# Kernel optimization log

Measured on AMD Instinct MI355X. Metric: run time of the kernel, lower is better.

Reference implementation:

```python
import jax, jax.numpy as jnp
import numpy as np

N_LOC, CONTENT, ADDR, HID, IN, OUT = 32768, 512, 64, 1024, 256, 10
OVERALL = CONTENT + ADDR   # 576
GRU_IN = IN + OVERALL      # 832
EPS = 1e-7


def setup_inputs() -> dict:
    key = jax.random.key(0)
    ks = jax.random.split(key, 16)
    def w(i, shape, scale=0.02):
        return jax.random.normal(ks[i], shape, jnp.float32) * scale
    return {
        "x": jax.random.normal(ks[0], (IN, 1), jnp.float32),
        "h0": jnp.zeros((HID, 1), jnp.float32),
        "memory_contents": w(1, (N_LOC, CONTENT)),
        "memory_addresses": w(2, (N_LOC, ADDR)),
        "W_query": w(3, (OVERALL, HID)),
        "b_query": jnp.zeros((OVERALL, 1), jnp.float32),
        "u_sharpen": w(4, (1, HID)),
        "b_sharpen": jnp.zeros((1, 1), jnp.float32),
        "u_lru": w(5, (1, HID)),
        "b_lru": jnp.zeros((1, 1), jnp.float32),
        "W_erase": w(6, (CONTENT, HID)),
        "b_erase": jnp.zeros((CONTENT, 1), jnp.float32),
        "W_content_hidden": w(7, (CONTENT, HID)),
        "W_content_input": w(8, (CONTENT, IN)),
        "b_content": jnp.zeros((CONTENT, 1), jnp.float32),
        "W_ih": w(9, (3 * HID, GRU_IN)),
        "W_hh": w(10, (3 * HID, HID)),
        "b_ih": jnp.zeros((3 * HID,), jnp.float32),
        "b_hh": jnp.zeros((3 * HID,), jnp.float32),
        "W_output": w(11, (OUT, HID)),
        "b_output": jnp.zeros((OUT, 1), jnp.float32),
        "num_addressing_steps": 8,
    }


def _dntm_forward(x, h0, memory_contents, memory_addresses, W_query, b_query,
                  u_sharpen, b_sharpen, u_lru, b_lru, W_erase, b_erase,
                  W_content_hidden, W_content_input, b_content,
                  W_ih, W_hh, b_ih, b_hh, W_output, b_output, num_steps):
    addr_norm_sq = jnp.sum(memory_addresses * memory_addresses, axis=1)  # (N,) constant across steps
    xcol = x[:, 0]

    def step(carry, _):
        h, mem, ema = carry  # h: (HID,1), mem: (N,CONTENT), ema: (N,)
        # --- address memory (content-based, sharpened, LRU-gated) ---
        query = (W_query @ h + b_query)[:, 0]                        # (OVERALL,)
        beta = jax.nn.softplus(u_sharpen @ h + b_sharpen)[0, 0] + 1.0
        full = jnp.concatenate([mem, memory_addresses], axis=1)      # (N, OVERALL) full memory view
        dots = full @ query                                          # (N,)
        row_norm = jnp.sqrt(jnp.sum(mem * mem, axis=1) + addr_norm_sq)
        sim = beta * dots / (row_norm * jnp.linalg.norm(query) + EPS)  # sharpened cosine sim (N,)
        gamma = jax.nn.sigmoid(u_lru @ h + b_lru)[0, 0]
        w_addr = jax.nn.softmax(sim - gamma * ema)                   # (N,)
        ema_new = 0.1 * ema + 0.9 * sim
        # --- read ---
        reading = full.T @ w_addr                                    # (OVERALL,)
        # --- GRU controller step (torch GRUCell math) ---
        gi = W_ih @ jnp.concatenate([xcol, reading]) + b_ih          # (3*HID,)
        gh = W_hh @ h[:, 0] + b_hh
        r = jax.nn.sigmoid(gi[:HID] + gh[:HID])
        z = jax.nn.sigmoid(gi[HID:2 * HID] + gh[HID:2 * HID])
        n = jnp.tanh(gi[2 * HID:] + r * gh[2 * HID:])
        h_new = ((1.0 - z) * n + z * h[:, 0])[:, None]               # (HID,1)
        # --- write/update memory: rank-1 erase + rank-1 add ---
        erase = jax.nn.sigmoid(W_erase @ h_new + b_erase)[:, 0]      # (CONTENT,)
        cand = jax.nn.relu(W_content_hidden @ h_new + W_content_input @ x + b_content)[:, 0]
        mem_new = mem * (1.0 - w_addr[:, None] * erase[None, :]) + w_addr[:, None] * cand[None, :]
        return (h_new, mem_new, ema_new), None

    ema0 = jnp.zeros((N_LOC,), memory_contents.dtype)
    (h, _, _), _ = jax.lax.scan(step, (h0, memory_contents, ema0), None, length=num_steps)
    output = jax.nn.log_softmax(W_output @ h + b_output, axis=0)     # (OUT,1)
    return h, output


def reference(x, h0, memory_contents, memory_addresses, W_query, b_query,
              u_sharpen, b_sharpen, u_lru, b_lru, W_erase, b_erase,
              W_content_hidden, W_content_input, b_content,
              W_ih, W_hh, b_ih, b_hh, W_output, b_output, num_addressing_steps):
    return _dntm_forward(x, h0, memory_contents, memory_addresses, W_query, b_query,
                         u_sharpen, b_sharpen, u_lru, b_lru, W_erase, b_erase,
                         W_content_hidden, W_content_input, b_content,
                         W_ih, W_hh, b_ih, b_hh, W_output, b_output, num_addressing_steps)
```

## Files before the change

kernel.cpp:

```cpp
#include <hip/hip_runtime.h>
#include <math.h>

#define N_LOC 32768
#define CONTENT 512
#define ADDR_D 64
#define HID 1024
#define IN_D 256
#define OUT_D 10
#define OVERALL 576
#define GRU_IN 832
#define EPS_C 1e-7f
#define NSTEPS 8

#define NBLK_P 2048
#define NWAVE_P (NBLK_P * 4)
#define RCOLS (OVERALL + 1)
#define RP 580
#define NRED 32

__device__ __forceinline__ float wred(float v) {
    #pragma unroll
    for (int m = 32; m; m >>= 1) v += __shfl_xor(v, m, 64);
    return v;
}
__device__ __forceinline__ float sigm(float x) { return 1.0f / (1.0f + expf(-x)); }
__device__ __forceinline__ float dot4(float4 a, float4 b) {
    return a.x * b.x + a.y * b.y + a.z * b.z + a.w * b.w;
}

__global__ __launch_bounds__(256) void k_init(const float* __restrict__ addrRows,
                                              float* __restrict__ addrsq,
                                              float* __restrict__ ema) {
    int tid = threadIdx.x, wid = tid >> 6, lane = tid & 63;
    int gid = blockIdx.x * 256 + tid;
    if (gid < N_LOC) ema[gid] = 0.0f;
    for (int i = blockIdx.x * 4 + wid; i < N_LOC; i += gridDim.x * 4) {
        float a = addrRows[(size_t)i * ADDR_D + lane];
        float sq = wred(a * a);
        if (lane == 0) addrsq[i] = sq;
    }
}

__global__ __launch_bounds__(256) void k_small(
    const float* __restrict__ W_e, const float* __restrict__ b_e,
    const float* __restrict__ W_ch, const float* __restrict__ W_ci, const float* __restrict__ b_c,
    const float* __restrict__ W_q, const float* __restrict__ b_q,
    const float* __restrict__ u_s, const float* __restrict__ u_l,
    const float* __restrict__ x, const float* __restrict__ h,
    float* __restrict__ erase, float* __restrict__ cand, float* __restrict__ query,
    float* __restrict__ slots_t, int doEC) {
    int tid = threadIdx.x, wid = tid >> 6, lane = tid & 63;
    int t = blockIdx.x * 4 + wid;
    const int base = doEC ? 2 * CONTENT : 0;
    const float4* h4 = (const float4*)h;
    const float4* x4 = (const float4*)x;
    if (doEC && t < CONTENT) {
        const float4* row = (const float4*)(W_e + (size_t)t * HID);
        float d = 0.0f;
        #pragma unroll
        for (int i = 0; i < 4; i++) d += dot4(row[lane + 64 * i], h4[lane + 64 * i]);
        d = wred(d);
        if (lane == 0) erase[t] = sigm(d + b_e[t]);
    } else if (doEC && t < 2 * CONTENT) {
        int r = t - CONTENT;
        const float4* row = (const float4*)(W_ch + (size_t)r * HID);
        float d = 0.0f;
        #pragma unroll
        for (int i = 0; i < 4; i++) d += dot4(row[lane + 64 * i], h4[lane + 64 * i]);
        const float4* row2 = (const float4*)(W_ci + (size_t)r * IN_D);
        d += dot4(row2[lane], x4[lane]);
        d = wred(d);
        if (lane == 0) cand[r] = fmaxf(d + b_c[r], 0.0f);
    } else if (t >= base && t < base + OVERALL) {
        int r = t - base;
        const float4* row = (const float4*)(W_q + (size_t)r * HID);
        float d = 0.0f;
        #pragma unroll
        for (int i = 0; i < 4; i++) d += dot4(row[lane + 64 * i], h4[lane + 64 * i]);
        d = wred(d);
        if (lane == 0) query[r] = d + b_q[r];
    } else if (t == base + OVERALL) {
        const float4* us4 = (const float4*)u_s;
        float d = 0.0f;
        #pragma unroll
        for (int i = 0; i < 4; i++) d += dot4(us4[lane + 64 * i], h4[lane + 64 * i]);
        d = wred(d);
        if (lane == 0) slots_t[1] = d;
    } else if (t == base + OVERALL + 1) {
        const float4* ul4 = (const float4*)u_l;
        float d = 0.0f;
        #pragma unroll
        for (int i = 0; i < 4; i++) d += dot4(ul4[lane + 64 * i], h4[lane + 64 * i]);
        d = wred(d);
        if (lane == 0) slots_t[2] = d;
    }
}

__global__ __launch_bounds__(256) void k_passAB(
    const float* __restrict__ memC,
    const float* __restrict__ addrRows, const float* __restrict__ query,
    const float* __restrict__ eraseAll, const float* __restrict__ candAll,
    const float* __restrict__ addrsq, float* __restrict__ ema,
    const float* __restrict__ expAll, float* __restrict__ exp_t,
    float* __restrict__ part,
    const float* __restrict__ slots_t, const float* __restrict__ ssum_red,
    const float* __restrict__ b_sh, const float* __restrict__ b_lr,
    int tstep) {
    int tid = threadIdx.x, wid = tid >> 6, lane = tid & 63;
    int gw = blockIdx.x * 4 + wid;
    const int i0 = gw;
    const int i1 = gw + NWAVE_P;
    const int i2 = gw + 2 * NWAVE_P;
    const int i3 = gw + 3 * NWAVE_P;

    __shared__ __align__(16) float lredw[4][RP];

    const float4* r0p = (const float4*)(memC + (size_t)i0 * CONTENT);
    const float4* r1p = (const float4*)(memC + (size_t)i1 * CONTENT);
    const float4* r2p = (const float4*)(memC + (size_t)i2 * CONTENT);
    const float4* r3p = (const float4*)(memC + (size_t)i3 * CONTENT);
    float4 m00 = r0p[lane], m01 = r0p[64 + lane];
    float4 m10 = r1p[lane], m11 = r1p[64 + lane];
    float4 m20 = r2p[lane], m21 = r2p[64 + lane];
    float4 m30 = r3p[lane], m31 = r3p[64 + lane];
    float av0 = addrRows[(size_t)i0 * ADDR_D + lane];
    float av1 = addrRows[(size_t)i1 * ADDR_D + lane];
    float av2 = addrRows[(size_t)i2 * ADDR_D + lane];
    float av3 = addrRows[(size_t)i3 * ADDR_D + lane];
    float eo0 = ema[i0], eo1 = ema[i1], eo2 = ema[i2], eo3 = ema[i3];
    float asq0 = addrsq[i0], asq1 = addrsq[i1], asq2 = addrsq[i2], asq3 = addrsq[i3];

    const float4 q0 = *(const float4*)(query + 4 * lane);
    const float4 q1 = *(const float4*)(query + 256 + 4 * lane);
    const float qa = query[512 + lane];
    const float qq = wred(dot4(q0, q0) + dot4(q1, q1) + qa * qa);
    const float qnorm = sqrtf(qq);
    const float bs = slots_t[1] + b_sh[0];
    const float beta = (bs > 20.0f ? bs : log1pf(expf(bs))) + 1.0f;
    const float gamma = sigm(slots_t[2] + b_lr[0]);

    #define UPD(m, e, c, wv) \
        m.x = m.x * (1.0f - wv * e.x) + wv * c.x; \
        m.y = m.y * (1.0f - wv * e.y) + wv * c.y; \
        m.z = m.z * (1.0f - wv * e.z) + wv * c.z; \
        m.w = m.w * (1.0f - wv * e.w) + wv * c.w;
    for (int u = 0; u < tstep; u++) {
        const float4 e0 = *(const float4*)(eraseAll + (size_t)u * CONTENT + 4 * lane);
        const float4 e1 = *(const float4*)(eraseAll + (size_t)u * CONTENT + 256 + 4 * lane);
        const float4 c0 = *(const float4*)(candAll + (size_t)u * CONTENT + 4 * lane);
        const float4 c1 = *(const float4*)(candAll + (size_t)u * CONTENT + 256 + 4 * lane);
        const float invp = 1.0f / ssum_red[u];
        const float* eb = expAll + (size_t)u * N_LOC;
        const float wv0 = eb[i0] * invp;
        const float wv1 = eb[i1] * invp;
        const float wv2 = eb[i2] * invp;
        const float wv3 = eb[i3] * invp;
        UPD(m00, e0, c0, wv0) UPD(m01, e1, c1, wv0)
        UPD(m10, e0, c0, wv1) UPD(m11, e1, c1, wv1)
        UPD(m20, e0, c0, wv2) UPD(m21, e1, c1, wv2)
        UPD(m30, e0, c0, wv3) UPD(m31, e1, c1, wv3)
    }
    #undef UPD

    float d0 = dot4(m00, q0) + dot4(m01, q1) + av0 * qa;
    float d1 = dot4(m10, q0) + dot4(m11, q1) + av1 * qa;
    float d2 = dot4(m20, q0) + dot4(m21, q1) + av2 * qa;
    float d3 = dot4(m30, q0) + dot4(m31, q1) + av3 * qa;
    float s0 = dot4(m00, m00) + dot4(m01, m01);
    float s1 = dot4(m10, m10) + dot4(m11, m11);
    float s2 = dot4(m20, m20) + dot4(m21, m21);
    float s3 = dot4(m30, m30) + dot4(m31, m31);
    #pragma unroll
    for (int m = 32; m; m >>= 1) {
        d0 += __shfl_xor(d0, m, 64); s0 += __shfl_xor(s0, m, 64);
        d1 += __shfl_xor(d1, m, 64); s1 += __shfl_xor(s1, m, 64);
        d2 += __shfl_xor(d2, m, 64); s2 += __shfl_xor(s2, m, 64);
        d3 += __shfl_xor(d3, m, 64); s3 += __shfl_xor(s3, m, 64);
    }
    float sim0 = beta * d0 / (sqrtf(s0 + asq0) * qnorm + EPS_C);
    float sim1 = beta * d1 / (sqrtf(s1 + asq1) * qnorm + EPS_C);
    float sim2 = beta * d2 / (sqrtf(s2 + asq2) * qnorm + EPS_C);
    float sim3 = beta * d3 / (sqrtf(s3 + asq3) * qnorm + EPS_C);
    float es0 = expf(sim0 - gamma * eo0);
    float es1 = expf(sim1 - gamma * eo1);
    float es2 = expf(sim2 - gamma * eo2);
    float es3 = expf(sim3 - gamma * eo3);
    if (lane == 0) {
        ema[i0] = 0.1f * eo0 + 0.9f * sim0;
        ema[i1] = 0.1f * eo1 + 0.9f * sim1;
        ema[i2] = 0.1f * eo2 + 0.9f * sim2;
        ema[i3] = 0.1f * eo3 + 0.9f * sim3;
        exp_t[i0] = es0; exp_t[i1] = es1; exp_t[i2] = es2; exp_t[i3] = es3;
    }

    float* lw = lredw[wid];
    #pragma unroll
    for (int k = 0; k < 4; k++) {
        float a = (k == 0) ? (es0 * m00.x + es1 * m10.x + es2 * m20.x + es3 * m30.x)
                : (k == 1) ? (es0 * m00.y + es1 * m10.y + es2 * m20.y + es3 * m30.y)
                : (k == 2) ? (es0 * m00.z + es1 * m10.z + es2 * m20.z + es3 * m30.z)
                           : (es0 * m00.w + es1 * m10.w + es2 * m20.w + es3 * m30.w);
        lw[4 * lane + k] = a;
        float b2 = (k == 0) ? (es0 * m01.x + es1 * m11.x + es2 * m21.x + es3 * m31.x)
                 : (k == 1) ? (es0 * m01.y + es1 * m11.y + es2 * m21.y + es3 * m31.y)
                 : (k == 2) ? (es0 * m01.z + es1 * m11.z + es2 * m21.z + es3 * m31.z)
                            : (es0 * m01.w + es1 * m11.w + es2 * m21.w + es3 * m31.w);
        lw[256 + 4 * lane + k] = b2;
    }
    lw[512 + lane] = es0 * av0 + es1 * av1 + es2 * av2 + es3 * av3;
    if (lane == 0) lw[576] = es0 + es1 + es2 + es3;
    __syncthreads();

    float* pb = part + (size_t)blockIdx.x * RP;
    for (int c = tid; c < RCOLS; c += 256)
        pb[c] = lredw[0][c] + lredw[1][c] + lredw[2][c] + lredw[3][c];
}

__global__ __launch_bounds__(256) void k_red(const float* __restrict__ part,
                                             float* __restrict__ partial2) {
    int tid = threadIdx.x;
    int g = blockIdx.x;
    float acc0 = 0.0f, acc1 = 0.0f, acc2 = 0.0f;
    const float* base = part + (size_t)g * 64 * RP;
    for (int r = 0; r < 64; r++) {
        const float* row = base + (size_t)r * RP;
        acc0 += row[tid];
        acc1 += row[256 + tid];
        if (tid < RCOLS - 512) acc2 += row[512 + tid];
    }
    partial2[(size_t)g * RP + tid] = acc0;
    partial2[(size_t)g * RP + 256 + tid] = acc1;
    if (tid < RCOLS - 512) partial2[(size_t)g * RP + 512 + tid] = acc2;
}

__global__ __launch_bounds__(256) void k_gru(
    const float* __restrict__ W_ih, const float* __restrict__ W_hh,
    const float* __restrict__ b_ih, const float* __restrict__ b_hh,
    const float* __restrict__ x, const float* __restrict__ partial2,
    float* __restrict__ ssum_red_t,
    const float* __restrict__ hcur, float* __restrict__ hnew) {
    int tid = threadIdx.x, wid = tid >> 6, lane = tid & 63;
    __shared__ __align__(16) float rs[OVERALL];
    __shared__ float ssum_sh;

    for (int c = tid; c < RCOLS; c += 256) {
        float s = 0.0f;
        #pragma unroll
        for (int g = 0; g < NRED; g++) s += partial2[(size_t)g * RP + c];
        if (c < OVERALL) rs[c] = s;
        else ssum_sh = s;
    }
    __syncthreads();
    if (blockIdx.x == 0 && tid == 0) ssum_red_t[0] = ssum_sh;

    const int k = blockIdx.x * 4 + wid;
    if (k >= HID) return;
    const float invs = 1.0f / ssum_sh;
    const float4* x4 = (const float4*)x;
    const float4* r4 = (const float4*)rs;
    const float4* h4 = (const float4*)hcur;
    const float4* Wi0 = (const float4*)(W_ih + (size_t)k * GRU_IN);
    const float4* Wi1 = (const float4*)(W_ih + (size_t)(k + HID) * GRU_IN);
    const float4* Wi2 = (const float4*)(W_ih + (size_t)(k + 2 * HID) * GRU_IN);
    float gi0 = 0, gi1 = 0, gi2 = 0;
    {
        float4 v = x4[lane];
        gi0 += dot4(Wi0[lane], v); gi1 += dot4(Wi1[lane], v); gi2 += dot4(Wi2[lane], v);
    }
    #pragma unroll
    for (int i = 0; i < 2; i++) {
        float4 v = r4[lane + 64 * i];
        v.x *= invs; v.y *= invs; v.z *= invs; v.w *= invs;
        gi0 += dot4(Wi0[64 + lane + 64 * i], v);
        gi1 += dot4(Wi1[64 + lane + 64 * i], v);
        gi2 += dot4(Wi2[64 + lane + 64 * i], v);
    }
    {
        int j = 768 + lane;
        float v = rs[512 + lane] * invs;
        gi0 += W_ih[(size_t)k * GRU_IN + j] * v;
        gi1 += W_ih[(size_t)(k + HID) * GRU_IN + j] * v;
        gi2 += W_ih[(size_t)(k + 2 * HID) * GRU_IN + j] * v;
    }
    const float4* Wh0 = (const float4*)(W_hh + (size_t)k * HID);
    const float4* Wh1 = (const float4*)(W_hh + (size_t)(k + HID) * HID);
    const float4* Wh2 = (const float4*)(W_hh + (size_t)(k + 2 * HID) * HID);
    float gh0 = 0, gh1 = 0, gh2 = 0;
    #pragma unroll
    for (int i = 0; i < 4; i++) {
        float4 v = h4[lane + 64 * i];
        gh0 += dot4(Wh0[lane + 64 * i], v);
        gh1 += dot4(Wh1[lane + 64 * i], v);
        gh2 += dot4(Wh2[lane + 64 * i], v);
    }
    gi0 = wred(gi0); gi1 = wred(gi1); gi2 = wred(gi2);
    gh0 = wred(gh0); gh1 = wred(gh1); gh2 = wred(gh2);
    if (lane == 0) {
        float r = sigm(gi0 + b_ih[k] + gh0 + b_hh[k]);
        float z = sigm(gi1 + b_ih[HID + k] + gh1 + b_hh[HID + k]);
        float n = tanhf(gi2 + b_ih[2 * HID + k] + r * (gh2 + b_hh[2 * HID + k]));
        hnew[k] = (1.0f - z) * n + z * hcur[k];
    }
}

__global__ __launch_bounds__(256) void k_out(const float* __restrict__ W_o,
                                             const float* __restrict__ b_o,
                                             const float* __restrict__ h,
                                             float* __restrict__ out) {
    int tid = threadIdx.x, wid = tid >> 6, lane = tid & 63;
    __shared__ float lg[OUT_D];
    for (int j = tid; j < HID; j += 256) out[j] = h[j];
    const float4* h4 = (const float4*)h;
    for (int u = wid; u < OUT_D; u += 4) {
        const float4* row = (const float4*)(W_o + (size_t)u * HID);
        float d = 0.0f;
        #pragma unroll
        for (int i = 0; i < 4; i++) d += dot4(row[lane + 64 * i], h4[lane + 64 * i]);
        d = wred(d);
        if (lane == 0) lg[u] = d + b_o[u];
    }
    __syncthreads();
    if (tid == 0) {
        float m = -1e30f;
        for (int u = 0; u < OUT_D; u++) m = fmaxf(m, lg[u]);
        float se = 0.0f;
        for (int u = 0; u < OUT_D; u++) se += expf(lg[u] - m);
        float lse = m + logf(se);
        for (int u = 0; u < OUT_D; u++) out[HID + u] = lg[u] - lse;
    }
}

extern "C" void kernel_launch(void* const* d_in, const int* in_sizes, int n_in,
                              void* d_out, int out_size, void* d_ws, size_t ws_size,
                              hipStream_t stream) {
    const float* x    = (const float*)d_in[0];
    const float* h0   = (const float*)d_in[1];
    const float* memC = (const float*)d_in[2];
    const float* addrR= (const float*)d_in[3];
    const float* W_q  = (const float*)d_in[4];
    const float* b_q  = (const float*)d_in[5];
    const float* u_s  = (const float*)d_in[6];
    const float* b_s  = (const float*)d_in[7];
    const float* u_l  = (const float*)d_in[8];
    const float* b_l  = (const float*)d_in[9];
    const float* W_e  = (const float*)d_in[10];
    const float* b_e  = (const float*)d_in[11];
    const float* W_ch = (const float*)d_in[12];
    const float* W_ci = (const float*)d_in[13];
    const float* b_c  = (const float*)d_in[14];
    const float* W_ih = (const float*)d_in[15];
    const float* W_hh = (const float*)d_in[16];
    const float* b_ih = (const float*)d_in[17];
    const float* b_hh = (const float*)d_in[18];
    const float* W_o  = (const float*)d_in[19];
    const float* b_o  = (const float*)d_in[20];

    const size_t SM_ADDRSQ = 0;
    const size_t SM_EXPA   = SM_ADDRSQ + N_LOC;
    const size_t SM_EMA    = SM_EXPA + (size_t)NSTEPS * N_LOC;
    const size_t SM_QUERY  = SM_EMA + N_LOC;
    const size_t SM_ER     = SM_QUERY + NSTEPS * OVERALL;
    const size_t SM_CAND   = SM_ER + NSTEPS * CONTENT;
    const size_t SM_H      = SM_CAND + NSTEPS * CONTENT;
    const size_t SM_SLOTS  = SM_H + (NSTEPS + 1) * HID;
    const size_t SM_SSUMR  = SM_SLOTS + NSTEPS * 8;
    const size_t SM_PART   = SM_SSUMR + 16;
    const size_t SM_PART2  = SM_PART + (size_t)NBLK_P * RP;

    float* sb = (float*)d_ws;
    float* addrsq  = sb + SM_ADDRSQ;
    float* exp_all = sb + SM_EXPA;
    float* ema     = sb + SM_EMA;
    float* query   = sb + SM_QUERY;
    float* erase   = sb + SM_ER;
    float* cand    = sb + SM_CAND;
    float* H       = sb + SM_H;
    float* slots   = sb + SM_SLOTS;
    float* ssum_red= sb + SM_SSUMR;
    float* part    = sb + SM_PART;
    float* partial2= sb + SM_PART2;

    k_init<<<512, 256, 0, stream>>>(addrR, addrsq, ema);
    k_small<<<(OVERALL + 2 + 3) / 4, 256, 0, stream>>>(
        W_e, b_e, W_ch, W_ci, b_c, W_q, b_q, u_s, u_l, x, h0,
        erase, cand, query, slots, 0);

    const float* hcur = h0;
    for (int t = 0; t < NSTEPS; t++) {
        k_passAB<<<NBLK_P, 256, 0, stream>>>(
            memC, addrR,
            query + t * OVERALL,
            erase, cand,
            addrsq, ema,
            exp_all, exp_all + (size_t)t * N_LOC,
            part,
            slots + t * 8, ssum_red, b_s, b_l,
            t);
        k_red<<<NRED, 256, 0, stream>>>(part, partial2);
        float* hn = H + (t + 1) * HID;
        k_gru<<<HID / 4, 256, 0, stream>>>(W_ih, W_hh, b_ih, b_hh, x,
                                           partial2, ssum_red + t, hcur, hn);
        if (t < NSTEPS - 1) {
            k_small<<<(2 * CONTENT + OVERALL + 2 + 3) / 4, 256, 0, stream>>>(
                W_e, b_e, W_ch, W_ci, b_c, W_q, b_q, u_s, u_l, x, hn,
                erase + t * CONTENT, cand + t * CONTENT,
                query + (t + 1) * OVERALL, slots + (t + 1) * 8, 1);
        }
        hcur = hn;
    }
    k_out<<<1, 256, 0, stream>>>(W_o, b_o, hcur, (float*)d_out);
}
```

Measured before the change: 602.0 us.

## Parallelize reduction, GRU and small matvecs across more blocks

The two-stage partial reduction (32 blocks, then every GRU block re-reducing 32 partials) becomes a single column-parallel reduction kernel that writes the final per-step read vector and softmax sum. The GRU kernel no longer recomputes that reduction in each block and uses one block per hidden unit, spreading each row dot product over 256 threads. The small matvec kernel likewise moves from one wave per row to one block per row. The aim is to cut the latency of the serial per-step small kernels by raising parallelism and removing redundant work, at the cost of more blocks and an extra LDS synchronisation.

```diff
diff --git a/kernel.cpp b/kernel.cpp
--- a/kernel.cpp
+++ b/kernel.cpp
@@ -16,7 +16,7 @@
 #define NWAVE_P (NBLK_P * 4)
 #define RCOLS (OVERALL + 1)
 #define RP 580
-#define NRED 32
+#define RSP 580
 
 __device__ __forceinline__ float wred(float v) {
     #pragma unroll
@@ -50,49 +50,43 @@
     float* __restrict__ erase, float* __restrict__ cand, float* __restrict__ query,
     float* __restrict__ slots_t, int doEC) {
     int tid = threadIdx.x, wid = tid >> 6, lane = tid & 63;
-    int t = blockIdx.x * 4 + wid;
-    const int base = doEC ? 2 * CONTENT : 0;
+    int r = blockIdx.x;
+    __shared__ float red[4];
+
+    int role, rr;
+    if (doEC) {
+        if (r < CONTENT)                { role = 0; rr = r; }
+        else if (r < 2 * CONTENT)       { role = 1; rr = r - CONTENT; }
+        else if (r < 2 * CONTENT + OVERALL) { role = 2; rr = r - 2 * CONTENT; }
+        else                            { role = 3 + (r - (2 * CONTENT + OVERALL)); rr = 0; }
+    } else {
+        if (r < OVERALL)                { role = 2; rr = r; }
+        else                            { role = 3 + (r - OVERALL); rr = 0; }
+    }
+
     const float4* h4 = (const float4*)h;
-    const float4* x4 = (const float4*)x;
-    if (doEC && t < CONTENT) {
-        const float4* row = (const float4*)(W_e + (size_t)t * HID);
-        float d = 0.0f;
-        #pragma unroll
-        for (int i = 0; i < 4; i++) d += dot4(row[lane + 64 * i], h4[lane + 64 * i]);
-        d = wred(d);
-        if (lane == 0) erase[t] = sigm(d + b_e[t]);
-    } else if (doEC && t < 2 * CONTENT) {
-        int r = t - CONTENT;
-        const float4* row = (const float4*)(W_ch + (size_t)r * HID);
-        float d = 0.0f;
-        #pragma unroll
-        for (int i = 0; i < 4; i++) d += dot4(row[lane + 64 * i], h4[lane + 64 * i]);
-        const float4* row2 = (const float4*)(W_ci + (size_t)r * IN_D);
-        d += dot4(row2[lane], x4[lane]);
-        d = wred(d);
-        if (lane == 0) cand[r] = fmaxf(d + b_c[r], 0.0f);
-    } else if (t >= base && t < base + OVERALL) {
-        int r = t - base;
-        const float4* row = (const float4*)(W_q + (size_t)r * HID);
-        float d = 0.0f;
-        #pragma unroll
-        for (int i = 0; i < 4; i++) d += dot4(row[lane + 64 * i], h4[lane + 64 * i]);
-        d = wred(d);
-        if (lane == 0) query[r] = d + b_q[r];
-    } else if (t == base + OVERALL) {
-        const float4* us4 = (const float4*)u_s;
-        float d = 0.0f;
-        #pragma unroll
-        for (int i = 0; i < 4; i++) d += dot4(us4[lane + 64 * i], h4[lane + 64 * i]);
-        d = wred(d);
-        if (lane == 0) slots_t[1] = d;
-    } else if (t == base + OVERALL + 1) {
-        const float4* ul4 = (const float4*)u_l;
-        float d = 0.0f;
-        #pragma unroll
-        for (int i = 0; i < 4; i++) d += dot4(ul4[lane + 64 * i], h4[lane + 64 * i]);
-        d = wred(d);
-        if (lane == 0) slots_t[2] = d;
+    const float4* row4;
+    if (role == 0)      row4 = (const float4*)(W_e  + (size_t)rr * HID);
+    else if (role == 1) row4 = (const float4*)(W_ch + (size_t)rr * HID);
+    else if (role == 2) row4 = (const float4*)(W_q  + (size_t)rr * HID);
+    else if (role == 3) row4 = (const float4*)u_s;
+    else                row4 = (const float4*)u_l;
+
+    float d = dot4(row4[tid], h4[tid]);
+    if (role == 1 && tid < 64) {
+        const float4* ci4 = (const float4*)(W_ci + (size_t)rr * IN_D);
+        d += dot4(ci4[tid], ((const float4*)x)[tid]);
+    }
+    d = wred(d);
+    if (lane == 0) red[wid] = d;
+    __syncthreads();
+    if (tid == 0) {
+        float s = red[0] + red[1] + red[2] + red[3];
+        if (role == 0)      erase[rr] = sigm(s + b_e[rr]);
+        else if (role == 1) cand[rr]  = fmaxf(s + b_c[rr], 0.0f);
+        else if (role == 2) query[rr] = s + b_q[rr];
+        else if (role == 3) slots_t[1] = s;
+        else                slots_t[2] = s;
     }
 }
 
@@ -102,8 +96,8 @@
     const float* __restrict__ eraseAll, const float* __restrict__ candAll,
     const float* __restrict__ addrsq, float* __restrict__ ema,
     const float* __restrict__ expAll, float* __restrict__ exp_t,
-    float* __restrict__ part,
-    const float* __restrict__ slots_t, const float* __restrict__ ssum_red,
+    float* __restrict__ part, const float* __restrict__ rsAll,
+    const float* __restrict__ slots_t,
     const float* __restrict__ b_sh, const float* __restrict__ b_lr,
     int tstep) {
     int tid = threadIdx.x, wid = tid >> 6, lane = tid & 63;
@@ -149,7 +143,7 @@
         const float4 e1 = *(const float4*)(eraseAll + (size_t)u * CONTENT + 256 + 4 * lane);
         const float4 c0 = *(const float4*)(candAll + (size_t)u * CONTENT + 4 * lane);
         const float4 c1 = *(const float4*)(candAll + (size_t)u * CONTENT + 256 + 4 * lane);
-        const float invp = 1.0f / ssum_red[u];
+        const float invp = 1.0f / rsAll[(size_t)u * RSP + OVERALL];
         const float* eb = expAll + (size_t)u * N_LOC;
         const float wv0 = eb[i0] * invp;
         const float wv1 = eb[i1] * invp;
@@ -216,89 +210,84 @@
         pb[c] = lredw[0][c] + lredw[1][c] + lredw[2][c] + lredw[3][c];
 }
 
-__global__ __launch_bounds__(256) void k_red(const float* __restrict__ part,
-                                             float* __restrict__ partial2) {
+__global__ __launch_bounds__(256) void k_redf(const float* __restrict__ part,
+                                              float* __restrict__ rs) {
     int tid = threadIdx.x;
-    int g = blockIdx.x;
-    float acc0 = 0.0f, acc1 = 0.0f, acc2 = 0.0f;
-    const float* base = part + (size_t)g * 64 * RP;
-    for (int r = 0; r < 64; r++) {
-        const float* row = base + (size_t)r * RP;
-        acc0 += row[tid];
-        acc1 += row[256 + tid];
-        if (tid < RCOLS - 512) acc2 += row[512 + tid];
-    }
-    partial2[(size_t)g * RP + tid] = acc0;
-    partial2[(size_t)g * RP + 256 + tid] = acc1;
-    if (tid < RCOLS - 512) partial2[(size_t)g * RP + 512 + tid] = acc2;
+    int cl = tid & 15;
+    int r0 = tid >> 4;
+    int c = blockIdx.x * 16 + cl;
+    __shared__ float lds[16][17];
+    float acc = 0.0f;
+    if (c < RCOLS) {
+        #pragma unroll 8
+        for (int r = r0; r < NBLK_P; r += 16)
+            acc += part[(size_t)r * RP + c];
+    }
+    lds[r0][cl] = acc;
+    __syncthreads();
+    if (tid < 16) {
+        int cc = blockIdx.x * 16 + tid;
+        if (cc < RCOLS) {
+            float s = 0.0f;
+            #pragma unroll
+            for (int g = 0; g < 16; g++) s += lds[g][tid];
+            rs[cc] = s;
+        }
+    }
 }
 
 __global__ __launch_bounds__(256) void k_gru(
     const float* __restrict__ W_ih, const float* __restrict__ W_hh,
     const float* __restrict__ b_ih, const float* __restrict__ b_hh,
-    const float* __restrict__ x, const float* __restrict__ partial2,
-    float* __restrict__ ssum_red_t,
+    const float* __restrict__ x, const float* __restrict__ rs,
     const float* __restrict__ hcur, float* __restrict__ hnew) {
     int tid = threadIdx.x, wid = tid >> 6, lane = tid & 63;
-    __shared__ __align__(16) float rs[OVERALL];
-    __shared__ float ssum_sh;
-
-    for (int c = tid; c < RCOLS; c += 256) {
-        float s = 0.0f;
-        #pragma unroll
-        for (int g = 0; g < NRED; g++) s += partial2[(size_t)g * RP + c];
-        if (c < OVERALL) rs[c] = s;
-        else ssum_sh = s;
-    }
-    __syncthreads();
-    if (blockIdx.x == 0 && tid == 0) ssum_red_t[0] = ssum_sh;
-
-    const int k = blockIdx.x * 4 + wid;
-    if (k >= HID) return;
-    const float invs = 1.0f / ssum_sh;
-    const float4* x4 = (const float4*)x;
-    const float4* r4 = (const float4*)rs;
-    const float4* h4 = (const float4*)hcur;
+    const int k = blockIdx.x;
+    __shared__ float red[4][6];
+
+    const float invs = 1.0f / rs[OVERALL];
     const float4* Wi0 = (const float4*)(W_ih + (size_t)k * GRU_IN);
     const float4* Wi1 = (const float4*)(W_ih + (size_t)(k + HID) * GRU_IN);
     const float4* Wi2 = (const float4*)(W_ih + (size_t)(k + 2 * HID) * GRU_IN);
-    float gi0 = 0, gi1 = 0, gi2 = 0;
-    {
-        float4 v = x4[lane];
-        gi0 += dot4(Wi0[lane], v); gi1 += dot4(Wi1[lane], v); gi2 += dot4(Wi2[lane], v);
-    }
-    #pragma unroll
-    for (int i = 0; i < 2; i++) {
-        float4 v = r4[lane + 64 * i];
-        v.x *= invs; v.y *= invs; v.z *= invs; v.w *= invs;
-        gi0 += dot4(Wi0[64 + lane + 64 * i], v);
-        gi1 += dot4(Wi1[64 + lane + 64 * i], v);
-        gi2 += dot4(Wi2[64 + lane + 64 * i], v);
-    }
-    {
-        int j = 768 + lane;
-        float v = rs[512 + lane] * invs;
-        gi0 += W_ih[(size_t)k * GRU_IN + j] * v;
-        gi1 += W_ih[(size_t)(k + HID) * GRU_IN + j] * v;
-        gi2 += W_ih[(size_t)(k + 2 * HID) * GRU_IN + j] * v;
-    }
     const float4* Wh0 = (const float4*)(W_hh + (size_t)k * HID);
     const float4* Wh1 = (const float4*)(W_hh + (size_t)(k + HID) * HID);
     const float4* Wh2 = (const float4*)(W_hh + (size_t)(k + 2 * HID) * HID);
-    float gh0 = 0, gh1 = 0, gh2 = 0;
+
+    float gi0 = 0, gi1 = 0, gi2 = 0;
+    if (tid < GRU_IN / 4) {
+        float4 v;
+        if (tid < IN_D / 4) v = ((const float4*)x)[tid];
+        else {
+            v = ((const float4*)rs)[tid - IN_D / 4];
+            v.x *= invs; v.y *= invs; v.z *= invs; v.w *= invs;
+        }
+        gi0 = dot4(Wi0[tid], v); gi1 = dot4(Wi1[tid], v); gi2 = dot4(Wi2[tid], v);
+    }
+    float4 hv = ((const float4*)hcur)[tid];
+    float gh0 = dot4(Wh0[tid], hv);
+    float gh1 = dot4(Wh1[tid], hv);
+    float gh2 = dot4(Wh2[tid], hv);
+
     #pragma unroll
-    for (int i = 0; i < 4; i++) {
-        float4 v = h4[lane + 64 * i];
-        gh0 += dot4(Wh0[lane + 64 * i], v);
-        gh1 += dot4(Wh1[lane + 64 * i], v);
-        gh2 += dot4(Wh2[lane + 64 * i], v);
-    }
-    gi0 = wred(gi0); gi1 = wred(gi1); gi2 = wred(gi2);
-    gh0 = wred(gh0); gh1 = wred(gh1); gh2 = wred(gh2);
+    for (int m = 32; m; m >>= 1) {
+        gi0 += __shfl_xor(gi0, m, 64); gi1 += __shfl_xor(gi1, m, 64); gi2 += __shfl_xor(gi2, m, 64);
+        gh0 += __shfl_xor(gh0, m, 64); gh1 += __shfl_xor(gh1, m, 64); gh2 += __shfl_xor(gh2, m, 64);
+    }
     if (lane == 0) {
-        float r = sigm(gi0 + b_ih[k] + gh0 + b_hh[k]);
-        float z = sigm(gi1 + b_ih[HID + k] + gh1 + b_hh[HID + k]);
-        float n = tanhf(gi2 + b_ih[2 * HID + k] + r * (gh2 + b_hh[2 * HID + k]));
+        red[wid][0] = gi0; red[wid][1] = gi1; red[wid][2] = gi2;
+        red[wid][3] = gh0; red[wid][4] = gh1; red[wid][5] = gh2;
+    }
+    __syncthreads();
+    if (tid == 0) {
+        float a0 = red[0][0] + red[1][0] + red[2][0] + red[3][0];
+        float a1 = red[0][1] + red[1][1] + red[2][1] + red[3][1];
+        float a2 = red[0][2] + red[1][2] + red[2][2] + red[3][2];
+        float a3 = red[0][3] + red[1][3] + red[2][3] + red[3][3];
+        float a4 = red[0][4] + red[1][4] + red[2][4] + red[3][4];
+        float a5 = red[0][5] + red[1][5] + red[2][5] + red[3][5];
+        float r = sigm(a0 + b_ih[k] + a3 + b_hh[k]);
+        float z = sigm(a1 + b_ih[HID + k] + a4 + b_hh[HID + k]);
+        float n = tanhf(a2 + b_ih[2 * HID + k] + r * (a5 + b_hh[2 * HID + k]));
         hnew[k] = (1.0f - z) * n + z * hcur[k];
     }
 }
@@ -363,9 +352,8 @@
     const size_t SM_CAND   = SM_ER + NSTEPS * CONTENT;
     const size_t SM_H      = SM_CAND + NSTEPS * CONTENT;
     const size_t SM_SLOTS  = SM_H + (NSTEPS + 1) * HID;
-    const size_t SM_SSUMR  = SM_SLOTS + NSTEPS * 8;
-    const size_t SM_PART   = SM_SSUMR + 16;
-    const size_t SM_PART2  = SM_PART + (size_t)NBLK_P * RP;
+    const size_t SM_RS     = SM_SLOTS + NSTEPS * 8;
+    const size_t SM_PART   = SM_RS + (size_t)NSTEPS * RSP;
 
     float* sb = (float*)d_ws;
     float* addrsq  = sb + SM_ADDRSQ;
@@ -376,12 +364,11 @@
     float* cand    = sb + SM_CAND;
     float* H       = sb + SM_H;
     float* slots   = sb + SM_SLOTS;
-    float* ssum_red= sb + SM_SSUMR;
+    float* rsAll   = sb + SM_RS;
     float* part    = sb + SM_PART;
-    float* partial2= sb + SM_PART2;
 
     k_init<<<512, 256, 0, stream>>>(addrR, addrsq, ema);
-    k_small<<<(OVERALL + 2 + 3) / 4, 256, 0, stream>>>(
+    k_small<<<OVERALL + 2, 256, 0, stream>>>(
         W_e, b_e, W_ch, W_ci, b_c, W_q, b_q, u_s, u_l, x, h0,
         erase, cand, query, slots, 0);
 
@@ -393,15 +380,16 @@
             erase, cand,
             addrsq, ema,
             exp_all, exp_all + (size_t)t * N_LOC,
-            part,
-            slots + t * 8, ssum_red, b_s, b_l,
+            part, rsAll,
+            slots + t * 8, b_s, b_l,
             t);
-        k_red<<<NRED, 256, 0, stream>>>(part, partial2);
+        float* rs_t = rsAll + (size_t)t * RSP;
+        k_redf<<<(RCOLS + 15) / 16, 256, 0, stream>>>(part, rs_t);
         float* hn = H + (t + 1) * HID;
-        k_gru<<<HID / 4, 256, 0, stream>>>(W_ih, W_hh, b_ih, b_hh, x,
-                                           partial2, ssum_red + t, hcur, hn);
+        k_gru<<<HID, 256, 0, stream>>>(W_ih, W_hh, b_ih, b_hh, x,
+                                       rs_t, hcur, hn);
         if (t < NSTEPS - 1) {
-            k_small<<<(2 * CONTENT + OVERALL + 2 + 3) / 4, 256, 0, stream>>>(
+            k_small<<<2 * CONTENT + OVERALL + 2, 256, 0, stream>>>(
                 W_e, b_e, W_ch, W_ci, b_c, W_q, b_q, u_s, u_l, x, hn,
                 erase + t * CONTENT, cand + t * CONTENT,
                 query + (t + 1) * OVERALL, slots + (t + 1) * 8, 1);
```

Measured after the change: 547.7 us. 9.0% less time.
